# Performance work log

Hardware: AMD Instinct MI355X
Metric: run time of the kernel (lower is better)

Reference implementation:

```python
import jax, jax.numpy as jnp
import numpy as np

UNITS, IN_DIM, CH = 256, 16, 2
R0, R1, R2 = 64, 8, 2
N = 262144


def setup_inputs() -> dict:
    key = jax.random.key(0)
    ks = jax.random.split(key, 7)
    inputs = jax.random.normal(ks[0], (N, IN_DIM), dtype=jnp.float32)
    core = jax.random.normal(ks[1], (R0, R1, R2), dtype=jnp.float32) * 0.1
    factor_0 = jax.random.normal(ks[2], (UNITS, R0), dtype=jnp.float32) * 0.1
    factor_1 = jax.random.normal(ks[3], (IN_DIM, R1), dtype=jnp.float32) * 0.1
    factor_2 = jax.random.normal(ks[4], (CH, R2), dtype=jnp.float32) * 0.1
    bias = jnp.zeros((UNITS, CH), dtype=jnp.float32)
    factor = jnp.ones((UNITS, CH), dtype=jnp.float32)
    return {"inputs": inputs, "core": core, "factor_0": factor_0,
            "factor_1": factor_1, "factor_2": factor_2, "bias": bias,
            "factor": factor}


def reference(inputs, core, factor_0, factor_1, factor_2, bias, factor):
    # Tucker reconstruction of kernel: (units, in_dim, channels)
    r0 = jnp.einsum('ijn,ki->kjn', core, factor_0)      # (units, r1, r2)
    r01 = jnp.einsum('ijn,kj->ikn', r0, factor_1)       # (units, in_dim, r2)
    kernel = jnp.einsum('ijn,kn->ijk', r01, factor_2)   # (units, in_dim, ch)
    # K.dot(inputs, kernel): contract inputs last dim with kernel dim -2
    out = jnp.einsum('bi,uic->buc', inputs, kernel)     # (N, units, ch)
    out = out + bias
    out = jnp.tanh(out) * factor
    out = jnp.sum(out, axis=-1)                          # (N, units)
    return out
```

## Files before the change

### kernel.cpp

```cpp
#include <hip/hip_runtime.h>

#define UNITS 256
#define IN_DIM 16
#define CH 2
#define R0C 64
#define R1C 8
#define R2C 2
#define NROWS 262144

#define NBLK 1024
#define K2LOG2E 2.8853900817779268f

typedef float v2f __attribute__((ext_vector_type(2)));
typedef float v4f __attribute__((ext_vector_type(4)));

#define UPACK 24
#define WS_FLOATS (UNITS * UPACK)

__device__ __forceinline__ void compute_unit_params(
    int u, const float* __restrict__ core, const float* __restrict__ f0,
    const float* __restrict__ f2, const float* __restrict__ bias,
    const float* __restrict__ fac, float wout[16], float aux[5]) {
    float r0[R1C][R2C] = {};
    #pragma unroll 8
    for (int a = 0; a < R0C; ++a) {
        float f0v = f0[u * R0C + a];
        #pragma unroll
        for (int j = 0; j < R1C; ++j)
            #pragma unroll
            for (int n = 0; n < R2C; ++n)
                r0[j][n] += f0v * core[(a * R1C + j) * R2C + n];
    }
    #pragma unroll
    for (int j = 0; j < R1C; ++j) {
        float w0 = r0[j][0] * f2[0 * R2C + 0] + r0[j][1] * f2[0 * R2C + 1];
        float w1 = r0[j][0] * f2[1 * R2C + 0] + r0[j][1] * f2[1 * R2C + 1];
        wout[j * 2 + 0] = w0 * K2LOG2E;
        wout[j * 2 + 1] = w1 * K2LOG2E;
    }
    float fc0 = fac[u * CH + 0], fc1 = fac[u * CH + 1];
    aux[0] = bias[u * CH + 0] * K2LOG2E;
    aux[1] = bias[u * CH + 1] * K2LOG2E;
    aux[2] = -2.0f * fc0;
    aux[3] = -2.0f * fc1;
    aux[4] = fc0 + fc1;
}

__global__ void wprep_kernel(const float* __restrict__ core,
                             const float* __restrict__ f0,
                             const float* __restrict__ f2,
                             const float* __restrict__ bias,
                             const float* __restrict__ fac,
                             float* __restrict__ ws) {
    int u = threadIdx.x;
    float w[16], aux[5];
    compute_unit_params(u, core, f0, f2, bias, fac, w, aux);
    float* p = ws + u * UPACK;
    #pragma unroll
    for (int k = 0; k < 16; ++k) p[k] = w[k];
    #pragma unroll
    for (int k = 0; k < 5; ++k) p[16 + k] = aux[k];
    p[21] = 0.f; p[22] = 0.f; p[23] = 0.f;
}

template <bool USE_WS>
__global__ __launch_bounds__(256) void mdense_main(
    const float* __restrict__ x,
    const float* __restrict__ f1,
    const float* __restrict__ wsbuf,
    const float* __restrict__ core, const float* __restrict__ f0,
    const float* __restrict__ f2, const float* __restrict__ bias,
    const float* __restrict__ fac,
    float* __restrict__ out)
{
    __shared__ float F1s[IN_DIM * R1C];
    const int tid = threadIdx.x;
    if (tid < 32)
        reinterpret_cast<float4*>(F1s)[tid] = reinterpret_cast<const float4*>(f1)[tid];
    __syncthreads();

    const int W = blockIdx.x * 4 + (tid >> 6);
    const int lane = tid & 63;
    const int u0 = lane * 4;

    v2f wv[4][R1C];
    v2f blv[4], mv[4];
    float gs[4];
    if (USE_WS) {
        #pragma unroll
        for (int q = 0; q < 4; ++q) {
            const float4* p4 = reinterpret_cast<const float4*>(wsbuf + (u0 + q) * UPACK);
            float4 w0 = p4[0], w1 = p4[1], w2 = p4[2], w3 = p4[3], a = p4[4];
            wv[q][0] = (v2f){w0.x, w0.y}; wv[q][1] = (v2f){w0.z, w0.w};
            wv[q][2] = (v2f){w1.x, w1.y}; wv[q][3] = (v2f){w1.z, w1.w};
            wv[q][4] = (v2f){w2.x, w2.y}; wv[q][5] = (v2f){w2.z, w2.w};
            wv[q][6] = (v2f){w3.x, w3.y}; wv[q][7] = (v2f){w3.z, w3.w};
            blv[q] = (v2f){a.x, a.y};
            mv[q]  = (v2f){a.z, a.w};
            gs[q] = wsbuf[(u0 + q) * UPACK + 20];
        }
    } else {
        for (int q = 0; q < 4; ++q) {
            float w[16], aux[5];
            compute_unit_params(u0 + q, core, f0, f2, bias, fac, w, aux);
            #pragma unroll
            for (int j = 0; j < R1C; ++j) wv[q][j] = (v2f){w[j * 2], w[j * 2 + 1]};
            blv[q] = (v2f){aux[0], aux[1]};
            mv[q]  = (v2f){aux[2], aux[3]};
            gs[q] = aux[4];
        }
    }

    const size_t rowbase = (size_t)W * 64;
    const float4* xp = reinterpret_cast<const float4*>(x + (rowbase + lane) * IN_DIM);
    float4 X0 = xp[0], X1 = xp[1], X2 = xp[2], X3 = xp[3];
    const float xs[16] = {X0.x, X0.y, X0.z, X0.w, X1.x, X1.y, X1.z, X1.w,
                          X2.x, X2.y, X2.z, X2.w, X3.x, X3.y, X3.z, X3.w};
    v2f Yv[4] = {(v2f){0.f, 0.f}, (v2f){0.f, 0.f}, (v2f){0.f, 0.f}, (v2f){0.f, 0.f}};
    #pragma unroll
    for (int i = 0; i < IN_DIM; ++i) {
        v2f xv = {xs[i], xs[i]};
        float4 ha = *reinterpret_cast<const float4*>(&F1s[i * R1C]);
        float4 hb = *reinterpret_cast<const float4*>(&F1s[i * R1C + 4]);
        Yv[0] += xv * (v2f){ha.x, ha.y};
        Yv[1] += xv * (v2f){ha.z, ha.w};
        Yv[2] += xv * (v2f){hb.x, hb.y};
        Yv[3] += xv * (v2f){hb.z, hb.w};
    }
    float yl[8] = {Yv[0][0], Yv[0][1], Yv[1][0], Yv[1][1],
                   Yv[2][0], Yv[2][1], Yv[3][0], Yv[3][1]};

    float* obase = out + rowbase * UNITS;
    #pragma unroll 2
    for (int r = 0; r < 64; ++r) {
        float yr[8];
        #pragma unroll
        for (int j = 0; j < R1C; ++j)
            yr[j] = __int_as_float(
                __builtin_amdgcn_readlane(__float_as_int(yl[j]), r));

        v2f acc0 = blv[0], acc1 = blv[1], acc2 = blv[2], acc3 = blv[3];
        #pragma unroll
        for (int j = 0; j < R1C; ++j) {
            v2f ys = {yr[j], yr[j]};
            acc0 += ys * wv[0][j];
            acc1 += ys * wv[1][j];
            acc2 += ys * wv[2][j];
            acc3 += ys * wv[3][j];
        }
        v4f o;
        {
            float e0 = __builtin_amdgcn_exp2f(acc0[0]);
            float e1 = __builtin_amdgcn_exp2f(acc0[1]);
            float r0 = __builtin_amdgcn_rcpf(1.0f + e0);
            float r1 = __builtin_amdgcn_rcpf(1.0f + e1);
            o.x = __builtin_fmaf(mv[0][0], r0, __builtin_fmaf(mv[0][1], r1, gs[0]));
        }
        {
            float e0 = __builtin_amdgcn_exp2f(acc1[0]);
            float e1 = __builtin_amdgcn_exp2f(acc1[1]);
            float r0 = __builtin_amdgcn_rcpf(1.0f + e0);
            float r1 = __builtin_amdgcn_rcpf(1.0f + e1);
            o.y = __builtin_fmaf(mv[1][0], r0, __builtin_fmaf(mv[1][1], r1, gs[1]));
        }
        {
            float e0 = __builtin_amdgcn_exp2f(acc2[0]);
            float e1 = __builtin_amdgcn_exp2f(acc2[1]);
            float r0 = __builtin_amdgcn_rcpf(1.0f + e0);
            float r1 = __builtin_amdgcn_rcpf(1.0f + e1);
            o.z = __builtin_fmaf(mv[2][0], r0, __builtin_fmaf(mv[2][1], r1, gs[2]));
        }
        {
            float e0 = __builtin_amdgcn_exp2f(acc3[0]);
            float e1 = __builtin_amdgcn_exp2f(acc3[1]);
            float r0 = __builtin_amdgcn_rcpf(1.0f + e0);
            float r1 = __builtin_amdgcn_rcpf(1.0f + e1);
            o.w = __builtin_fmaf(mv[3][0], r0, __builtin_fmaf(mv[3][1], r1, gs[3]));
        }
        v4f* p4 = reinterpret_cast<v4f*>(obase + (size_t)r * UNITS) + lane;
        __builtin_nontemporal_store(o, p4);
    }
}

extern "C" void kernel_launch(void* const* d_in, const int* in_sizes, int n_in,
                              void* d_out, int out_size, void* d_ws, size_t ws_size,
                              hipStream_t stream) {
    const float* x    = (const float*)d_in[0];
    const float* core = (const float*)d_in[1];
    const float* f0   = (const float*)d_in[2];
    const float* f1   = (const float*)d_in[3];
    const float* f2   = (const float*)d_in[4];
    const float* bias = (const float*)d_in[5];
    const float* fac  = (const float*)d_in[6];
    float* out = (float*)d_out;

    if (ws_size >= WS_FLOATS * sizeof(float)) {
        float* ws = (float*)d_ws;
        wprep_kernel<<<1, 256, 0, stream>>>(core, f0, f2, bias, fac, ws);
        mdense_main<true><<<NBLK, 256, 0, stream>>>(x, f1, ws, core, f0, f2,
                                                    bias, fac, out);
    } else {
        mdense_main<false><<<NBLK, 256, 0, stream>>>(x, f1, nullptr, core, f0,
                                                     f2, bias, fac, out);
    }
}
```

Measured before the change: 67.49 us.

## Fuse per-unit weight prep into main kernel via shared memory

Drops the separate single-block prep kernel and its global workspace. Each block now has every thread compute one unit's Tucker-reconstructed parameters into a 24 KB shared array, then each lane reads its four units from shared memory. This removes a kernel launch and the serial dependency on a tiny one-block kernel. In exchange every one of the 1024 blocks repeats the 64-step reduction per unit, and shared-memory use per block rises, which may cap occupancy. Launch bounds now also ask for four blocks per CU.

```diff
diff --git a/kernel.cpp b/kernel.cpp
--- a/kernel.cpp
+++ b/kernel.cpp
@@ -15,7 +15,6 @@
 typedef float v4f __attribute__((ext_vector_type(4)));
 
 #define UPACK 24
-#define WS_FLOATS (UNITS * UPACK)
 
 __device__ __forceinline__ void compute_unit_params(
     int u, const float* __restrict__ core, const float* __restrict__ f0,
@@ -46,37 +45,32 @@
     aux[4] = fc0 + fc1;
 }
 
-__global__ void wprep_kernel(const float* __restrict__ core,
-                             const float* __restrict__ f0,
-                             const float* __restrict__ f2,
-                             const float* __restrict__ bias,
-                             const float* __restrict__ fac,
-                             float* __restrict__ ws) {
-    int u = threadIdx.x;
-    float w[16], aux[5];
-    compute_unit_params(u, core, f0, f2, bias, fac, w, aux);
-    float* p = ws + u * UPACK;
-    #pragma unroll
-    for (int k = 0; k < 16; ++k) p[k] = w[k];
-    #pragma unroll
-    for (int k = 0; k < 5; ++k) p[16 + k] = aux[k];
-    p[21] = 0.f; p[22] = 0.f; p[23] = 0.f;
-}
-
-template <bool USE_WS>
-__global__ __launch_bounds__(256) void mdense_main(
+__global__ __launch_bounds__(256, 4) void mdense_main(
     const float* __restrict__ x,
     const float* __restrict__ f1,
-    const float* __restrict__ wsbuf,
     const float* __restrict__ core, const float* __restrict__ f0,
     const float* __restrict__ f2, const float* __restrict__ bias,
     const float* __restrict__ fac,
     float* __restrict__ out)
 {
     __shared__ float F1s[IN_DIM * R1C];
+    __shared__ float P[UNITS * UPACK];
+
     const int tid = threadIdx.x;
     if (tid < 32)
         reinterpret_cast<float4*>(F1s)[tid] = reinterpret_cast<const float4*>(f1)[tid];
+
+    {
+        float w[16], aux[5];
+        compute_unit_params(tid, core, f0, f2, bias, fac, w, aux);
+        float* p = &P[tid * UPACK];
+        reinterpret_cast<float4*>(p)[0] = make_float4(w[0], w[1], w[2], w[3]);
+        reinterpret_cast<float4*>(p)[1] = make_float4(w[4], w[5], w[6], w[7]);
+        reinterpret_cast<float4*>(p)[2] = make_float4(w[8], w[9], w[10], w[11]);
+        reinterpret_cast<float4*>(p)[3] = make_float4(w[12], w[13], w[14], w[15]);
+        reinterpret_cast<float4*>(p)[4] = make_float4(aux[0], aux[1], aux[2], aux[3]);
+        p[20] = aux[4];
+    }
     __syncthreads();
 
     const int W = blockIdx.x * 4 + (tid >> 6);
@@ -86,29 +80,21 @@
     v2f wv[4][R1C];
     v2f blv[4], mv[4];
     float gs[4];
-    if (USE_WS) {
-        #pragma unroll
-        for (int q = 0; q < 4; ++q) {
-            const float4* p4 = reinterpret_cast<const float4*>(wsbuf + (u0 + q) * UPACK);
-            float4 w0 = p4[0], w1 = p4[1], w2 = p4[2], w3 = p4[3], a = p4[4];
-            wv[q][0] = (v2f){w0.x, w0.y}; wv[q][1] = (v2f){w0.z, w0.w};
-            wv[q][2] = (v2f){w1.x, w1.y}; wv[q][3] = (v2f){w1.z, w1.w};
-            wv[q][4] = (v2f){w2.x, w2.y}; wv[q][5] = (v2f){w2.z, w2.w};
-            wv[q][6] = (v2f){w3.x, w3.y}; wv[q][7] = (v2f){w3.z, w3.w};
-            blv[q] = (v2f){a.x, a.y};
-            mv[q]  = (v2f){a.z, a.w};
-            gs[q] = wsbuf[(u0 + q) * UPACK + 20];
-        }
-    } else {
-        for (int q = 0; q < 4; ++q) {
-            float w[16], aux[5];
-            compute_unit_params(u0 + q, core, f0, f2, bias, fac, w, aux);
-            #pragma unroll
-            for (int j = 0; j < R1C; ++j) wv[q][j] = (v2f){w[j * 2], w[j * 2 + 1]};
-            blv[q] = (v2f){aux[0], aux[1]};
-            mv[q]  = (v2f){aux[2], aux[3]};
-            gs[q] = aux[4];
-        }
+    #pragma unroll
+    for (int q = 0; q < 4; ++q) {
+        const float* p = &P[(u0 + q) * UPACK];
+        float4 w0 = reinterpret_cast<const float4*>(p)[0];
+        float4 w1 = reinterpret_cast<const float4*>(p)[1];
+        float4 w2 = reinterpret_cast<const float4*>(p)[2];
+        float4 w3 = reinterpret_cast<const float4*>(p)[3];
+        float4 a  = reinterpret_cast<const float4*>(p)[4];
+        wv[q][0] = (v2f){w0.x, w0.y}; wv[q][1] = (v2f){w0.z, w0.w};
+        wv[q][2] = (v2f){w1.x, w1.y}; wv[q][3] = (v2f){w1.z, w1.w};
+        wv[q][4] = (v2f){w2.x, w2.y}; wv[q][5] = (v2f){w2.z, w2.w};
+        wv[q][6] = (v2f){w3.x, w3.y}; wv[q][7] = (v2f){w3.z, w3.w};
+        blv[q] = (v2f){a.x, a.y};
+        mv[q]  = (v2f){a.z, a.w};
+        gs[q] = p[20];
     }
 
     const size_t rowbase = (size_t)W * 64;
@@ -194,13 +180,5 @@
     const float* fac  = (const float*)d_in[6];
     float* out = (float*)d_out;
 
-    if (ws_size >= WS_FLOATS * sizeof(float)) {
-        float* ws = (float*)d_ws;
-        wprep_kernel<<<1, 256, 0, stream>>>(core, f0, f2, bias, fac, ws);
-        mdense_main<true><<<NBLK, 256, 0, stream>>>(x, f1, ws, core, f0, f2,
-                                                    bias, fac, out);
-    } else {
-        mdense_main<false><<<NBLK, 256, 0, stream>>>(x, f1, nullptr, core, f0,
-                                                     f2, bias, fac, out);
-    }
+    mdense_main<<<NBLK, 256, 0, stream>>>(x, f1, core, f0, f2, bias, fac, out);
 }
```

Result: slower. 70.13 us (+3.9%).
